# Optimization experiments

Measured on AMD Instinct MI355X. Metric: run time of the kernel, lower is better.

Reference implementation:

```python
import jax, jax.numpy as jnp
import numpy as np

N, H, E = 40000, 128, 640000
BN_EPS = 1e-5


def setup_inputs() -> dict:
    key = jax.random.key(0)
    ks = jax.random.split(key, 5)
    x = jax.random.normal(ks[0], (N, H), dtype=jnp.float32)
    edge_index = jax.random.randint(ks[1], (2, E), 0, N, dtype=jnp.int64)
    eps = jnp.zeros((1,), dtype=jnp.float32)
    s = 1.0 / np.sqrt(H)  # torch Linear init scale
    W1 = jax.random.uniform(ks[2], (H, H), jnp.float32, -s, s)
    b1 = jnp.zeros((H,), dtype=jnp.float32)
    W2 = jax.random.uniform(ks[3], (H, H), jnp.float32, -s, s)
    b2 = jnp.zeros((H,), dtype=jnp.float32)
    gamma = jnp.ones((H,), dtype=jnp.float32)
    beta = jnp.zeros((H,), dtype=jnp.float32)
    return {"x": x, "edge_index": edge_index, "eps": eps,
            "W1": W1, "b1": b1, "W2": W2, "b2": b2,
            "gamma": gamma, "beta": beta}


def reference(x, edge_index, eps, W1, b1, W2, b2, gamma, beta):
    src = edge_index[0]
    tgt = edge_index[1]
    # gather source features, scatter-add into target rows: [N, H]
    agg = jax.ops.segment_sum(x[src], tgt, num_segments=x.shape[0])
    out = agg + (1.0 + eps) * x
    # MLP: Linear -> ReLU -> Linear -> BatchNorm1d (train mode) -> ReLU
    h = jax.nn.relu(out @ W1.T + b1)
    h = h @ W2.T + b2
    mean = jnp.mean(h, axis=0)
    var = jnp.mean((h - mean) ** 2, axis=0)  # biased var, as BN uses
    h = (h - mean) * jax.lax.rsqrt(var + BN_EPS) * gamma + beta
    return jax.nn.relu(h)
```

## Files before the change

kernel.cpp:

```cpp
#include <hip/hip_runtime.h>

#define HDIM 128
#define BN_EPS 1e-5f
#define SCAN_BINS 1024
#define NPART 8
#define LSTR 136
#define MROWS 16
#define NREP 8

typedef short short8 __attribute__((ext_vector_type(8)));
typedef float floatx4 __attribute__((ext_vector_type(4)));

__device__ __forceinline__ unsigned short f2b(float f) {
    union { float f; unsigned u; } v; v.f = f;
    unsigned r = v.u + 0x7FFFu + ((v.u >> 16) & 1u);
    return (unsigned short)(r >> 16);
}

__device__ __forceinline__ float b2f(unsigned short b) {
    union { unsigned u; float f; } v; v.u = (unsigned)b << 16;
    return v.f;
}

__global__ __launch_bounds__(256) void prep_kernel(
    const float* __restrict__ x, unsigned short* __restrict__ xB, long n4,
    const float* __restrict__ W1, const float* __restrict__ W2,
    unsigned short* __restrict__ W1B, unsigned short* __restrict__ W2B,
    const int* __restrict__ eidx, int* __restrict__ hist,
    int* __restrict__ rank, int E)
{
    int tid = blockIdx.x * 256 + threadIdx.x;
    int stride = gridDim.x * 256;
    for (long i = tid; i < n4; i += stride) {
        float4 v = ((const float4*)x)[i];
        ushort4 o;
        o.x = f2b(v.x); o.y = f2b(v.y); o.z = f2b(v.z); o.w = f2b(v.w);
        ((ushort4*)xB)[i] = o;
    }
    for (int i = tid; i < HDIM * HDIM; i += stride) {
        W1B[i] = f2b(W1[i]);
        W2B[i] = f2b(W2[i]);
    }
    for (int e = tid; e < E; e += stride) {
        rank[e] = atomicAdd(&hist[eidx[E + e]], 1);
    }
}

__global__ __launch_bounds__(256) void block_scan_kernel(
    const int* __restrict__ hist, int* __restrict__ offsets,
    int* __restrict__ blockSums, float* __restrict__ statSum, int N)
{
    __shared__ int ts[256];
    int b = blockIdx.x, t = threadIdx.x;
    if (b == 0) {
        for (int i = t; i < 2 * NREP * HDIM; i += 256) statSum[i] = 0.f;
    }
    int base = b * SCAN_BINS + t * 4;
    int4 h = make_int4(0, 0, 0, 0);
    if (base + 3 < N) {
        h = *(const int4*)(hist + base);
    } else {
        if (base + 0 < N) h.x = hist[base + 0];
        if (base + 1 < N) h.y = hist[base + 1];
        if (base + 2 < N) h.z = hist[base + 2];
    }
    int s = h.x + h.y + h.z + h.w;
    ts[t] = s;
    __syncthreads();
    for (int off = 1; off < 256; off <<= 1) {
        int v = ts[t];
        int add = (t >= off) ? ts[t - off] : 0;
        __syncthreads();
        ts[t] = v + add;
        __syncthreads();
    }
    int excl = ts[t] - s;
    int4 o;
    o.x = excl;
    o.y = o.x + h.x;
    o.z = o.y + h.y;
    o.w = o.z + h.z;
    if (base + 3 < N) {
        *(int4*)(offsets + base) = o;
    } else {
        if (base + 0 < N) offsets[base + 0] = o.x;
        if (base + 1 < N) offsets[base + 1] = o.y;
        if (base + 2 < N) offsets[base + 2] = o.z;
    }
    if (t == 255) blockSums[b] = ts[255];
}

__global__ __launch_bounds__(256) void scan_finalize_kernel(
    const int* __restrict__ blockSums, int* __restrict__ offsets, int N, int NB)
{
    __shared__ int ts[256];
    int b = blockIdx.x, t = threadIdx.x;
    ts[t] = (t < NB) ? blockSums[t] : 0;
    __syncthreads();
    for (int off = 1; off < 256; off <<= 1) {
        int v = ts[t];
        int add = (t >= off) ? ts[t - off] : 0;
        __syncthreads();
        ts[t] = v + add;
        __syncthreads();
    }
    int prefix = (b == 0) ? 0 : ts[b - 1];
    if (b == 0 && t == 0) offsets[N] = ts[NB - 1];
    int base = b * SCAN_BINS + t * 4;
    if (base + 3 < N) {
        int4 o = *(int4*)(offsets + base);
        o.x += prefix; o.y += prefix; o.z += prefix; o.w += prefix;
        *(int4*)(offsets + base) = o;
    } else {
        for (int j = 0; j < 4; j++) {
            int i = base + j;
            if (i < N) offsets[i] += prefix;
        }
    }
}

__global__ __launch_bounds__(256) void reorder_kernel(
    const int* __restrict__ eidx, const int* __restrict__ offsets,
    const int* __restrict__ rank, int* __restrict__ srcSorted,
    int E, int partSize)
{
    int part = blockIdx.x & (NPART - 1);
    int bi = blockIdx.x >> 3;
    int nb = gridDim.x >> 3;
    int lo = part * partSize;
    int hi = lo + partSize;
    int stride = nb * 256;
    for (int e = bi * 256 + threadIdx.x; e < E; e += stride) {
        int t = eidx[E + e];
        if (t >= lo && t < hi) {
            srcSorted[offsets[t] + rank[e]] = eidx[e];
        }
    }
}

__global__ __launch_bounds__(256, 8) void mega_kernel(
    const float* __restrict__ x, const unsigned short* __restrict__ xB,
    const int* __restrict__ offsets, const int* __restrict__ srcSorted,
    const float* __restrict__ eps,
    const unsigned short* __restrict__ W1B, const float* __restrict__ b1,
    const unsigned short* __restrict__ W2B, const float* __restrict__ b2,
    float* __restrict__ out, float* __restrict__ statSum,
    float* __restrict__ statSqs, int N)
{
    __shared__ unsigned short sA[MROWS * LSTR];
    __shared__ unsigned short sH[MROWS * LSTR];

    int tid = threadIdx.x;
    int rb = blockIdx.x * MROWS;

    float coef = 1.0f + eps[0];
    int tx = tid & 15, ty = tid >> 4;
    int col = tx * 8;
    {
        int row = rb + ty;
        float acc[8] = {0.f, 0.f, 0.f, 0.f, 0.f, 0.f, 0.f, 0.f};
        if (row < N) {
            float4 xv0 = *(const float4*)(x + (size_t)row * HDIM + col);
            float4 xv1 = *(const float4*)(x + (size_t)row * HDIM + col + 4);
            acc[0] = coef * xv0.x; acc[1] = coef * xv0.y;
            acc[2] = coef * xv0.z; acc[3] = coef * xv0.w;
            acc[4] = coef * xv1.x; acc[5] = coef * xv1.y;
            acc[6] = coef * xv1.z; acc[7] = coef * xv1.w;
            int beg = offsets[row], end = offsets[row + 1];
            int e = beg;
            for (; e + 7 < end; e += 8) {
                short8 u[8];
                #pragma unroll
                for (int q = 0; q < 8; q++) {
                    int s = srcSorted[e + q];
                    u[q] = *(const short8*)(xB + (size_t)s * HDIM + col);
                }
                #pragma unroll
                for (int q = 0; q < 8; q++)
                    #pragma unroll
                    for (int j = 0; j < 8; j++)
                        acc[j] += b2f((unsigned short)u[q][j]);
            }
            for (; e + 3 < end; e += 4) {
                short8 u[4];
                #pragma unroll
                for (int q = 0; q < 4; q++) {
                    int s = srcSorted[e + q];
                    u[q] = *(const short8*)(xB + (size_t)s * HDIM + col);
                }
                #pragma unroll
                for (int q = 0; q < 4; q++)
                    #pragma unroll
                    for (int j = 0; j < 8; j++)
                        acc[j] += b2f((unsigned short)u[q][j]);
            }
            for (; e < end; e++) {
                int s = srcSorted[e];
                short8 u = *(const short8*)(xB + (size_t)s * HDIM + col);
                #pragma unroll
                for (int j = 0; j < 8; j++)
                    acc[j] += b2f((unsigned short)u[j]);
            }
        }
        short8 o;
        #pragma unroll
        for (int j = 0; j < 8; j++) o[j] = (short)f2b(acc[j]);
        *(short8*)(sA + ty * LSTR + col) = o;
    }
    __syncthreads();

    int w = tid >> 6;
    int l = tid & 63;
    int m = l & 15, quad = l >> 4;
    int cbase = w * 32;

    floatx4 acc1[2];
    #pragma unroll
    for (int t = 0; t < 2; t++) acc1[t] = (floatx4){0.f, 0.f, 0.f, 0.f};
    #pragma unroll
    for (int kk = 0; kk < 4; kk++) {
        int k0 = kk * 32 + quad * 8;
        short8 a = *(const short8*)(sA + m * LSTR + k0);
        #pragma unroll
        for (int t = 0; t < 2; t++) {
            short8 bfr = *(const short8*)(W1B + (size_t)(cbase + t * 16 + m) * HDIM + k0);
            acc1[t] = __builtin_amdgcn_mfma_f32_16x16x32_bf16(a, bfr, acc1[t], 0, 0, 0);
        }
    }
    #pragma unroll
    for (int t = 0; t < 2; t++) {
        int colc = cbase + t * 16 + m;
        float bs = b1[colc];
        #pragma unroll
        for (int r = 0; r < 4; r++) {
            float v = fmaxf(acc1[t][r] + bs, 0.f);
            sH[(quad * 4 + r) * LSTR + colc] = f2b(v);
        }
    }
    __syncthreads();

    floatx4 acc2[2];
    #pragma unroll
    for (int t = 0; t < 2; t++) acc2[t] = (floatx4){0.f, 0.f, 0.f, 0.f};
    #pragma unroll
    for (int kk = 0; kk < 4; kk++) {
        int k0 = kk * 32 + quad * 8;
        short8 a = *(const short8*)(sH + m * LSTR + k0);
        #pragma unroll
        for (int t = 0; t < 2; t++) {
            short8 bfr = *(const short8*)(W2B + (size_t)(cbase + t * 16 + m) * HDIM + k0);
            acc2[t] = __builtin_amdgcn_mfma_f32_16x16x32_bf16(a, bfr, acc2[t], 0, 0, 0);
        }
    }
    float* repSum = statSum + (blockIdx.x & (NREP - 1)) * HDIM;
    float* repSqs = statSqs + (blockIdx.x & (NREP - 1)) * HDIM;
    int row0 = rb + quad * 4;
    #pragma unroll
    for (int t = 0; t < 2; t++) {
        int colc = cbase + t * 16 + m;
        float bs = b2[colc];
        float cs = 0.f, cq = 0.f;
        #pragma unroll
        for (int r = 0; r < 4; r++) {
            int row = row0 + r;
            if (row < N) {
                float v = acc2[t][r] + bs;
                out[(size_t)row * HDIM + colc] = v;
                cs += v; cq += v * v;
            }
        }
        cs += __shfl_xor(cs, 16, 64);
        cs += __shfl_xor(cs, 32, 64);
        cq += __shfl_xor(cq, 16, 64);
        cq += __shfl_xor(cq, 32, 64);
        if (quad == 0) {
            atomicAdd(&repSum[colc], cs);
            atomicAdd(&repSqs[colc], cq);
        }
    }
}

__global__ __launch_bounds__(256) void bn_apply_kernel(
    float* __restrict__ out, const float* __restrict__ statSum,
    const float* __restrict__ statSqs, const float* __restrict__ gamma,
    const float* __restrict__ beta, int N, long n4)
{
    __shared__ float sSc[HDIM];
    __shared__ float sSh[HDIM];
    int t = threadIdx.x;
    if (t < HDIM) {
        float s = 0.f, q = 0.f;
        #pragma unroll
        for (int r = 0; r < NREP; r++) {
            s += statSum[r * HDIM + t];
            q += statSqs[r * HDIM + t];
        }
        float invN = 1.0f / (float)N;
        float mean = s * invN;
        float var = q * invN - mean * mean;
        float sc = gamma[t] * rsqrtf(var + BN_EPS);
        sSc[t] = sc;
        sSh[t] = beta[t] - mean * sc;
    }
    __syncthreads();
    long stride = (long)gridDim.x * 256;
    for (long i = (long)blockIdx.x * 256 + t; i < n4; i += stride) {
        int cg = (int)(i & 31) * 4;
        float4 v = ((float4*)out)[i];
        v.x = fmaxf(v.x * sSc[cg + 0] + sSh[cg + 0], 0.f);
        v.y = fmaxf(v.y * sSc[cg + 1] + sSh[cg + 1], 0.f);
        v.z = fmaxf(v.z * sSc[cg + 2] + sSh[cg + 2], 0.f);
        v.w = fmaxf(v.w * sSc[cg + 3] + sSh[cg + 3], 0.f);
        ((float4*)out)[i] = v;
    }
}

extern "C" void kernel_launch(void* const* d_in, const int* in_sizes, int n_in,
                              void* d_out, int out_size, void* d_ws, size_t ws_size,
                              hipStream_t stream) {
    const float* x     = (const float*)d_in[0];
    const int*   eidx  = (const int*)d_in[1];
    const float* eps   = (const float*)d_in[2];
    const float* W1    = (const float*)d_in[3];
    const float* b1    = (const float*)d_in[4];
    const float* W2    = (const float*)d_in[5];
    const float* b2    = (const float*)d_in[6];
    const float* gamma = (const float*)d_in[7];
    const float* beta  = (const float*)d_in[8];
    float* out = (float*)d_out;

    int N = in_sizes[0] / HDIM;
    int E = in_sizes[1] / 2;
    size_t NH = (size_t)N * HDIM;
    int NB = (N + SCAN_BINS - 1) / SCAN_BINS;
    int NpadOff = (N + 1 + 3) & ~3;
    int partSize = (N + NPART - 1) / NPART;
    long n4 = (long)NH / 4;

    unsigned short* xB   = (unsigned short*)d_ws;
    unsigned short* W1B  = xB + NH;
    unsigned short* W2B  = W1B + HDIM * HDIM;
    float* statSum = (float*)(W2B + HDIM * HDIM);
    float* statSqs = statSum + NREP * HDIM;
    int*   hist    = (int*)(statSqs + NREP * HDIM);
    int*   offsets = hist + N;
    int*   rank    = offsets + NpadOff;
    int*   srcSorted = rank + E;
    int*   blockSums = srcSorted + E;

    hipMemsetAsync(hist, 0, (size_t)N * sizeof(int), stream);
    prep_kernel<<<1280, 256, 0, stream>>>(x, xB, n4, W1, W2, W1B, W2B, eidx, hist, rank, E);
    block_scan_kernel<<<NB, 256, 0, stream>>>(hist, offsets, blockSums, statSum, N);
    scan_finalize_kernel<<<NB, 256, 0, stream>>>(blockSums, offsets, N, NB);
    reorder_kernel<<<2048, 256, 0, stream>>>(eidx, offsets, rank, srcSorted, E, partSize);
    int gblocks = (N + MROWS - 1) / MROWS;
    mega_kernel<<<gblocks, 256, 0, stream>>>(
        x, xB, offsets, srcSorted, eps, W1B, b1, W2B, b2,
        out, statSum, statSqs, N);
    bn_apply_kernel<<<2048, 256, 0, stream>>>(
        out, statSum, statSqs, gamma, beta, N, n4);
}
```

Baseline: 184.1 us.

## Pad CSR segments to multiples of eight with a zero dummy row

Result: faster. 177.0 us (-3.9%).

```diff
diff --git a/kernel.cpp b/kernel.cpp
--- a/kernel.cpp
+++ b/kernel.cpp
@@ -27,10 +27,14 @@
     const float* __restrict__ W1, const float* __restrict__ W2,
     unsigned short* __restrict__ W1B, unsigned short* __restrict__ W2B,
     const int* __restrict__ eidx, int* __restrict__ hist,
-    int* __restrict__ rank, int E)
+    int* __restrict__ rank, int E, int N)
 {
     int tid = blockIdx.x * 256 + threadIdx.x;
     int stride = gridDim.x * 256;
+    if (blockIdx.x == 0 && threadIdx.x < 32) {
+        ushort4 z; z.x = 0; z.y = 0; z.z = 0; z.w = 0;
+        ((ushort4*)(xB + (size_t)N * HDIM))[threadIdx.x] = z;
+    }
     for (long i = tid; i < n4; i += stride) {
         float4 v = ((const float4*)x)[i];
         ushort4 o;
@@ -41,7 +45,18 @@
         W1B[i] = f2b(W1[i]);
         W2B[i] = f2b(W2[i]);
     }
-    for (int e = tid; e < E; e += stride) {
+    int E4 = E >> 2;
+    const int4* tgt4 = (const int4*)(eidx + E);
+    for (int e4 = tid; e4 < E4; e4 += stride) {
+        int4 t = tgt4[e4];
+        int4 r;
+        r.x = atomicAdd(&hist[t.x], 1);
+        r.y = atomicAdd(&hist[t.y], 1);
+        r.z = atomicAdd(&hist[t.z], 1);
+        r.w = atomicAdd(&hist[t.w], 1);
+        ((int4*)rank)[e4] = r;
+    }
+    for (int e = E4 * 4 + tid; e < E; e += stride) {
         rank[e] = atomicAdd(&hist[eidx[E + e]], 1);
     }
 }
@@ -64,7 +79,12 @@
         if (base + 1 < N) h.y = hist[base + 1];
         if (base + 2 < N) h.z = hist[base + 2];
     }
-    int s = h.x + h.y + h.z + h.w;
+    int4 p;
+    p.x = (h.x + 7) & ~7;
+    p.y = (h.y + 7) & ~7;
+    p.z = (h.z + 7) & ~7;
+    p.w = (h.w + 7) & ~7;
+    int s = p.x + p.y + p.z + p.w;
     ts[t] = s;
     __syncthreads();
     for (int off = 1; off < 256; off <<= 1) {
@@ -77,9 +97,9 @@
     int excl = ts[t] - s;
     int4 o;
     o.x = excl;
-    o.y = o.x + h.x;
-    o.z = o.y + h.y;
-    o.w = o.z + h.z;
+    o.y = o.x + p.x;
+    o.z = o.y + p.y;
+    o.w = o.z + p.z;
     if (base + 3 < N) {
         *(int4*)(offsets + base) = o;
     } else {
@@ -91,7 +111,8 @@
 }
 
 __global__ __launch_bounds__(256) void scan_finalize_kernel(
-    const int* __restrict__ blockSums, int* __restrict__ offsets, int N, int NB)
+    const int* __restrict__ blockSums, int* __restrict__ offsets,
+    const int* __restrict__ hist, int* __restrict__ srcSorted, int N, int NB)
 {
     __shared__ int ts[256];
     int b = blockIdx.x, t = threadIdx.x;
@@ -111,10 +132,20 @@
         int4 o = *(int4*)(offsets + base);
         o.x += prefix; o.y += prefix; o.z += prefix; o.w += prefix;
         *(int4*)(offsets + base) = o;
+        int4 h = *(const int4*)(hist + base);
+        for (int p = o.x + h.x; p < o.x + ((h.x + 7) & ~7); p++) srcSorted[p] = N;
+        for (int p = o.y + h.y; p < o.y + ((h.y + 7) & ~7); p++) srcSorted[p] = N;
+        for (int p = o.z + h.z; p < o.z + ((h.z + 7) & ~7); p++) srcSorted[p] = N;
+        for (int p = o.w + h.w; p < o.w + ((h.w + 7) & ~7); p++) srcSorted[p] = N;
     } else {
         for (int j = 0; j < 4; j++) {
             int i = base + j;
-            if (i < N) offsets[i] += prefix;
+            if (i < N) {
+                int o = offsets[i] + prefix;
+                offsets[i] = o;
+                int h = hist[i];
+                for (int p = o + h; p < o + ((h + 7) & ~7); p++) srcSorted[p] = N;
+            }
         }
     }
 }
@@ -166,40 +197,28 @@
             acc[2] = coef * xv0.z; acc[3] = coef * xv0.w;
             acc[4] = coef * xv1.x; acc[5] = coef * xv1.y;
             acc[6] = coef * xv1.z; acc[7] = coef * xv1.w;
-            int beg = offsets[row], end = offsets[row + 1];
-            int e = beg;
-            for (; e + 7 < end; e += 8) {
+            int beg = offsets[row];
+            int nb = (offsets[row + 1] - beg) >> 3;
+            const int4* sp = (const int4*)(srcSorted + beg);
+            int4 ia, ib;
+            if (nb > 0) { ia = sp[0]; ib = sp[1]; }
+            for (int b = 0; b < nb; b++) {
                 short8 u[8];
-                #pragma unroll
-                for (int q = 0; q < 8; q++) {
-                    int s = srcSorted[e + q];
-                    u[q] = *(const short8*)(xB + (size_t)s * HDIM + col);
-                }
+                u[0] = *(const short8*)(xB + (size_t)ia.x * HDIM + col);
+                u[1] = *(const short8*)(xB + (size_t)ia.y * HDIM + col);
+                u[2] = *(const short8*)(xB + (size_t)ia.z * HDIM + col);
+                u[3] = *(const short8*)(xB + (size_t)ia.w * HDIM + col);
+                u[4] = *(const short8*)(xB + (size_t)ib.x * HDIM + col);
+                u[5] = *(const short8*)(xB + (size_t)ib.y * HDIM + col);
+                u[6] = *(const short8*)(xB + (size_t)ib.z * HDIM + col);
+                u[7] = *(const short8*)(xB + (size_t)ib.w * HDIM + col);
+                sp += 2;
+                if (b + 1 < nb) { ia = sp[0]; ib = sp[1]; }
                 #pragma unroll
                 for (int q = 0; q < 8; q++)
                     #pragma unroll
                     for (int j = 0; j < 8; j++)
                         acc[j] += b2f((unsigned short)u[q][j]);
-            }
-            for (; e + 3 < end; e += 4) {
-                short8 u[4];
-                #pragma unroll
-                for (int q = 0; q < 4; q++) {
-                    int s = srcSorted[e + q];
-                    u[q] = *(const short8*)(xB + (size_t)s * HDIM + col);
-                }
-                #pragma unroll
-                for (int q = 0; q < 4; q++)
-                    #pragma unroll
-                    for (int j = 0; j < 8; j++)
-                        acc[j] += b2f((unsigned short)u[q][j]);
-            }
-            for (; e < end; e++) {
-                int s = srcSorted[e];
-                short8 u = *(const short8*)(xB + (size_t)s * HDIM + col);
-                #pragma unroll
-                for (int j = 0; j < 8; j++)
-                    acc[j] += b2f((unsigned short)u[j]);
             }
         }
         short8 o;
@@ -336,9 +355,10 @@
     int NpadOff = (N + 1 + 3) & ~3;
     int partSize = (N + NPART - 1) / NPART;
     long n4 = (long)NH / 4;
+    int Emax = E + 7 * N + 64;
 
     unsigned short* xB   = (unsigned short*)d_ws;
-    unsigned short* W1B  = xB + NH;
+    unsigned short* W1B  = xB + NH + HDIM;
     unsigned short* W2B  = W1B + HDIM * HDIM;
     float* statSum = (float*)(W2B + HDIM * HDIM);
     float* statSqs = statSum + NREP * HDIM;
@@ -346,12 +366,12 @@
     int*   offsets = hist + N;
     int*   rank    = offsets + NpadOff;
     int*   srcSorted = rank + E;
-    int*   blockSums = srcSorted + E;
+    int*   blockSums = srcSorted + Emax;
 
     hipMemsetAsync(hist, 0, (size_t)N * sizeof(int), stream);
-    prep_kernel<<<1280, 256, 0, stream>>>(x, xB, n4, W1, W2, W1B, W2B, eidx, hist, rank, E);
+    prep_kernel<<<1280, 256, 0, stream>>>(x, xB, n4, W1, W2, W1B, W2B, eidx, hist, rank, E, N);
     block_scan_kernel<<<NB, 256, 0, stream>>>(hist, offsets, blockSums, statSum, N);
-    scan_finalize_kernel<<<NB, 256, 0, stream>>>(blockSums, offsets, N, NB);
+    scan_finalize_kernel<<<NB, 256, 0, stream>>>(blockSums, offsets, hist, srcSorted, N, NB);
     reorder_kernel<<<2048, 256, 0, stream>>>(eidx, offsets, rank, srcSorted, E, partSize);
     int gblocks = (N + MROWS - 1) / MROWS;
     mega_kernel<<<gblocks, 256, 0, stream>>>(
```
